# Kernel tuning notes

Measured on AMD Instinct MI355X. Metric: run time of the kernel, lower is better.

## Reference

```python
import jax, jax.numpy as jnp
import numpy as np

S, P, H, E = 32, 32, 128, 64        # scenes, peds/scene, h_dim, embedding_dim
B1, B2 = 512, 1024                  # mlp_pre_pool hidden, bottleneck_dim
M1 = 1024                           # decoder mlp hidden
N = S * P
T = 12                              # seq_len (decode horizon)
BN_INV = 1.0 / np.sqrt(1.0 + 1e-5)  # eval-mode BatchNorm, running mean=0 var=1


def setup_inputs() -> dict:
    key = jax.random.key(0)
    ks = jax.random.split(key, 32)
    rn = lambda k, sh, s=0.05: jax.random.normal(k, sh, dtype=jnp.float32) * s
    inp = {
        'last_pos': rn(ks[0], (N, 2), 1.0),
        'last_pos_rel': rn(ks[1], (N, 2), 1.0),
        'h0': rn(ks[2], (N, H), 0.1),
        'c0': rn(ks[3], (N, H), 0.1),
        'seq_start_end': jnp.stack([jnp.arange(S) * P, (jnp.arange(S) + 1) * P], 1).astype(jnp.int32),
        # decoder spatial embedding Linear(2, E)
        'emb_W': rn(ks[4], (E, 2)), 'emb_b': rn(ks[5], (E,)),
        # LSTM (torch gate order i,f,g,o)
        'lstm_Wih': rn(ks[6], (4 * H, E)), 'lstm_Whh': rn(ks[7], (4 * H, H)),
        'lstm_bih': rn(ks[8], (4 * H,)), 'lstm_bhh': rn(ks[9], (4 * H,)),
        # hidden2pos Linear(H, 2)
        'pos_W': rn(ks[10], (2, H)), 'pos_b': rn(ks[11], (2,)),
        # pool_net spatial embedding Linear(2, E)
        'sp_W': rn(ks[12], (E, 2)), 'sp_b': rn(ks[13], (E,)),
        # mlp_pre_pool: Linear(E+H, 512)+BN+ReLU, Linear(512, 1024)+BN+ReLU
        'pp1_W': rn(ks[14], (B1, E + H)), 'pp1_b': rn(ks[15], (B1,)),
        'pp1_g': 1.0 + rn(ks[16], (B1,)), 'pp1_be': rn(ks[17], (B1,)),
        'pp2_W': rn(ks[18], (B2, B1)), 'pp2_b': rn(ks[19], (B2,)),
        'pp2_g': 1.0 + rn(ks[20], (B2,)), 'pp2_be': rn(ks[21], (B2,)),
        # decoder mlp: Linear(H+1024, 1024)+BN+ReLU, Linear(1024, H)+BN+ReLU
        'm1_W': rn(ks[22], (M1, H + B2)), 'm1_b': rn(ks[23], (M1,)),
        'm1_g': 1.0 + rn(ks[24], (M1,)), 'm1_be': rn(ks[25], (M1,)),
        'm2_W': rn(ks[26], (H, M1)), 'm2_b': rn(ks[27], (H,)),
        'm2_g': 1.0 + rn(ks[28], (H,)), 'm2_be': rn(ks[29], (H,)),
    }
    return inp


def _bn(x, g, b):
    return x * BN_INV * g + b


def reference(last_pos, last_pos_rel, h0, c0, seq_start_end,
              emb_W, emb_b, lstm_Wih, lstm_Whh, lstm_bih, lstm_bhh,
              pos_W, pos_b, sp_W, sp_b,
              pp1_W, pp1_b, pp1_g, pp1_be, pp2_W, pp2_b, pp2_g, pp2_be,
              m1_W, m1_b, m1_g, m1_be, m2_W, m2_b, m2_g, m2_be):
    # seq_start_end encodes uniform scenes of size P; pooling is done per scene.
    def step(carry, _):
        h, c, lp, din = carry  # h,c:[N,H]  lp:[N,2]  din:[N,E]
        gates = din @ lstm_Wih.T + lstm_bih + h @ lstm_Whh.T + lstm_bhh
        i, f, g_, o = jnp.split(gates, 4, axis=-1)
        c2 = jax.nn.sigmoid(f) * c + jax.nn.sigmoid(i) * jnp.tanh(g_)
        h2 = jax.nn.sigmoid(o) * jnp.tanh(c2)
        rel_pos = h2 @ pos_W.T + pos_b          # [N,2]
        curr = rel_pos + lp                     # [N,2]
        # ---- PoolHiddenNet: per-scene all-pairs gather -> MLP -> max ----
        ps = curr.reshape(S, P, 2)
        rel = ps[:, None, :, :] - ps[:, :, None, :]   # [s,i,j] = pos_j - pos_i
        rel = rel / jnp.maximum(jnp.linalg.norm(rel, axis=-1, keepdims=True), 1e-12)
        emb = rel @ sp_W.T + sp_b                      # [S,P,P,E]
        hj = jnp.broadcast_to(h2.reshape(S, 1, P, H), (S, P, P, H))
        x = jnp.concatenate([emb, hj], -1)             # [S,P,P,E+H]
        x = jax.nn.relu(_bn(x @ pp1_W.T + pp1_b, pp1_g, pp1_be))
        x = jax.nn.relu(_bn(x @ pp2_W.T + pp2_b, pp2_g, pp2_be))
        pool = x.max(axis=2).reshape(N, B2)            # max over neighbours j
        # ---- hidden refinement MLP ----
        dh = jnp.concatenate([h2, pool], 1)
        dh = jax.nn.relu(_bn(dh @ m1_W.T + m1_b, m1_g, m1_be))
        dh = jax.nn.relu(_bn(dh @ m2_W.T + m2_b, m2_g, m2_be))
        din2 = rel_pos @ emb_W.T + emb_b
        return (dh, c2, curr, din2), rel_pos

    din0 = last_pos_rel @ emb_W.T + emb_b
    _, preds = jax.lax.scan(step, (h0, c0, last_pos, din0), None, length=T)
    return preds  # [T, N, 2] predicted relative displacements
```

## Files before the change

### kernel.cpp

```cpp
#include <hip/hip_runtime.h>
#include <hip/hip_bf16.h>
#include <math.h>

#define DEVFN __device__ __forceinline__

constexpr float BN_INV = 0.99999500003749971f;

DEVFN float sigm(float x) { return 1.0f / (1.0f + expf(-x)); }

DEVFN unsigned short f2bf(float f) {
    __hip_bfloat16 b = __float2bfloat16(f);
    return *reinterpret_cast<unsigned short*>(&b);
}
DEVFN float bf2f(unsigned short u) {
    unsigned int x = ((unsigned int)u) << 16;
    return *reinterpret_cast<float*>(&x);
}
DEVFN void splitf(float v, unsigned short& h, unsigned short& l) {
    h = f2bf(v);
    l = f2bf(v - bf2f(h));
}
DEVFN unsigned int pack2(unsigned short a, unsigned short b) {
    return (unsigned int)a | ((unsigned int)b << 16);
}

typedef __attribute__((ext_vector_type(8))) short short8;
typedef __attribute__((ext_vector_type(4))) float f32x4;

#define ASYNC_COPY16(gsrc, ldst)                                                            \
    __builtin_amdgcn_global_load_lds((const __attribute__((address_space(1))) unsigned int*)(gsrc), \
                                     (__attribute__((address_space(3))) unsigned int*)(ldst), 16, 0, 0)


__global__ void pre_misc(
    const float* __restrict__ Wih, const float* __restrict__ Whh,
    const float* __restrict__ bih, const float* __restrict__ bhh,
    float* __restrict__ WgT, float* __restrict__ bg,
    const float* __restrict__ pp1W, const float* __restrict__ pp1g,
    float* __restrict__ Wh1T,
    const float* __restrict__ spW, const float* __restrict__ spb,
    const float* __restrict__ pp1b, const float* __restrict__ pp1be,
    float* __restrict__ Mp, float* __restrict__ c1,
    const float* __restrict__ lp, const float* __restrict__ lpr,
    const float* __restrict__ h0, const float* __restrict__ c0,
    const float* __restrict__ embW, const float* __restrict__ embb,
    float* __restrict__ h_st, float* __restrict__ c_st,
    float* __restrict__ curr, float* __restrict__ din) {
    int bid = blockIdx.x, t = threadIdx.x;
    if (bid < 384) {
        int idx = bid * 256 + t;
        int k = idx >> 9, tt = idx & 511;
        WgT[idx] = (k < 64) ? Wih[tt * 64 + k] : Whh[tt * 128 + (k - 64)];
        if (idx < 512) bg[idx] = bih[idx] + bhh[idx];
    } else if (bid < 640) {
        int idx = (bid - 384) * 256 + t;
        int h = idx >> 9, k = idx & 511;
        Wh1T[idx] = pp1W[k * 192 + 64 + h] * (BN_INV * pp1g[k]);
    } else if (bid < 642) {
        int k = (bid - 640) * 256 + t;
        float m0 = 0.f, m1 = 0.f, c0v = 0.f;
        for (int e = 0; e < 64; e++) {
            float w = pp1W[k * 192 + e];
            m0 += spW[e * 2] * w; m1 += spW[e * 2 + 1] * w; c0v += spb[e] * w;
        }
        float s = BN_INV * pp1g[k];
        Mp[k] = m0 * s; Mp[512 + k] = m1 * s;
        c1[k] = (c0v + pp1b[k]) * s + pp1be[k];
    } else {
        int idx = (bid - 642) * 256 + t;
        h_st[idx] = h0[idx];
        c_st[idx] = c0[idx];
        if (idx < 1024 * 2) curr[idx] = lp[idx];
        if (idx < 1024 * 64) {
            int n = idx >> 6, e = idx & 63;
            din[idx] = fmaf(lpr[n * 2], embW[e * 2], fmaf(lpr[n * 2 + 1], embW[e * 2 + 1], embb[e]));
        }
    }
}

__global__ void pre_w2bf(const float* __restrict__ W, const float* __restrict__ b,
                         const float* __restrict__ g, const float* __restrict__ be,
                         unsigned short* __restrict__ Wbf, float* __restrict__ cv, int swz) {
    int idx = blockIdx.x * blockDim.x + threadIdx.x;
    int ko = idx >> 9, k = idx & 511;
    float s = BN_INV * g[ko];
    int outk = swz ? ((k & ~63) | ((((k >> 3) & 7) ^ (ko & 7)) << 3) | (k & 7)) : k;
    Wbf[(ko << 9) + outk] = f2bf(W[idx] * s);
    if (idx < 1024) cv[idx] = b[idx] * s + be[idx];
}

__global__ void pre_w1split(const float* __restrict__ W, const float* __restrict__ b,
                            const float* __restrict__ g, const float* __restrict__ be,
                            unsigned short* __restrict__ Wh, unsigned short* __restrict__ Wl,
                            float* __restrict__ cv) {
    int idx = blockIdx.x * blockDim.x + threadIdx.x;
    int ko = idx / 1152;
    float s = BN_INV * g[ko];
    unsigned short h, l;
    splitf(W[idx] * s, h, l);
    Wh[idx] = h; Wl[idx] = l;
    if (idx < 1024) {
        float s2 = BN_INV * g[idx];
        cv[idx] = b[idx] * s2 + be[idx];
    }
}

__global__ void pre_w2split(const float* __restrict__ W, const float* __restrict__ b,
                            const float* __restrict__ g, const float* __restrict__ be,
                            unsigned short* __restrict__ Wh, unsigned short* __restrict__ Wl,
                            float* __restrict__ cv) {
    int idx = blockIdx.x * blockDim.x + threadIdx.x;
    int ko = idx >> 10;
    float s = BN_INV * g[ko];
    unsigned short h, l;
    splitf(W[idx] * s, h, l);
    Wh[idx] = h; Wl[idx] = l;
    if (idx < 128) {
        float s2 = BN_INV * g[idx];
        cv[idx] = b[idx] * s2 + be[idx];
    }
}


__global__ __launch_bounds__(512) void k_lstm(
    const float* __restrict__ WgT, const float* __restrict__ bg,
    float* __restrict__ h_st, float* __restrict__ c_st,
    float* __restrict__ din, float* __restrict__ curr,
    unsigned short* __restrict__ h2h, unsigned short* __restrict__ h2l,
    const float* __restrict__ posW, const float* __restrict__ posb,
    const float* __restrict__ embW, const float* __restrict__ embb,
    const float* __restrict__ Wh1T, const float* __restrict__ c1,
    float* __restrict__ Hp, int doHp,
    float* __restrict__ preds) {
    int n0 = blockIdx.x << 2;
    int t = threadIdx.x;
    __shared__ float xs[4][256];
    __shared__ float gates[4][512];
    __shared__ float h2s[4][128];
    __shared__ float rp[4][2];
#pragma unroll
    for (int u = 0; u < 2; u++) {
        int lin = t + (u << 9);
        int r = lin >> 8, k = lin & 255;
        float v = 0.f;
        if (k < 64) v = din[(n0 + r) * 64 + k];
        else if (k < 192) v = h_st[(n0 + r) * 128 + (k - 64)];
        xs[r][k] = v;
    }
    __syncthreads();
    float a0 = bg[t], a1 = a0, a2 = a0, a3 = a0;
#pragma unroll 4
    for (int k = 0; k < 192; k++) {
        float w = WgT[(k << 9) + t];
        a0 = fmaf(xs[0][k], w, a0);
        a1 = fmaf(xs[1][k], w, a1);
        a2 = fmaf(xs[2][k], w, a2);
        a3 = fmaf(xs[3][k], w, a3);
    }
    gates[0][t] = a0; gates[1][t] = a1; gates[2][t] = a2; gates[3][t] = a3;
    __syncthreads();
    {
        int r = t >> 7, hx = t & 127;
        float ig = sigm(gates[r][hx]);
        float fg = sigm(gates[r][128 + hx]);
        float gg = tanhf(gates[r][256 + hx]);
        float og = sigm(gates[r][384 + hx]);
        float c2 = fmaf(fg, c_st[(n0 + r) * 128 + hx], ig * gg);
        float h2 = og * tanhf(c2);
        c_st[(n0 + r) * 128 + hx] = c2;
        unsigned short sh, sl;
        splitf(h2, sh, sl);
        h2h[(n0 + r) * 128 + hx] = sh;
        h2l[(n0 + r) * 128 + hx] = sl;
        h2s[r][hx] = h2;
    }
    __syncthreads();
    int wv = t >> 6, l = t & 63;
    if (wv < 4) {
        float p0 = fmaf(h2s[wv][l], posW[l], h2s[wv][l + 64] * posW[l + 64]);
        float p1 = fmaf(h2s[wv][l], posW[128 + l], h2s[wv][l + 64] * posW[192 + l]);
#pragma unroll
        for (int off = 32; off > 0; off >>= 1) {
            p0 += __shfl_down(p0, off, 64);
            p1 += __shfl_down(p1, off, 64);
        }
        if (l == 0) { rp[wv][0] = p0 + posb[0]; rp[wv][1] = p1 + posb[1]; }
    }
    __syncthreads();
    if (t < 256) {
        int r = t >> 6, e = t & 63;
        float r0 = rp[r][0], r1 = rp[r][1];
        din[(n0 + r) * 64 + e] = fmaf(r0, embW[e * 2], fmaf(r1, embW[e * 2 + 1], embb[e]));
        if (e == 0) {
            preds[(n0 + r) * 2] = r0; preds[(n0 + r) * 2 + 1] = r1;
            curr[(n0 + r) * 2] += r0; curr[(n0 + r) * 2 + 1] += r1;
        }
    }
    if (doHp) {
        float cc = c1[t];
        float q0 = cc, q1 = cc, q2 = cc, q3 = cc;
#pragma unroll 4
        for (int h = 0; h < 128; h++) {
            float w = Wh1T[(h << 9) + t];
            q0 = fmaf(h2s[0][h], w, q0);
            q1 = fmaf(h2s[1][h], w, q1);
            q2 = fmaf(h2s[2][h], w, q2);
            q3 = fmaf(h2s[3][h], w, q3);
        }
        Hp[((n0 + 0) << 9) + t] = q0;
        Hp[((n0 + 1) << 9) + t] = q1;
        Hp[((n0 + 2) << 9) + t] = q2;
        Hp[((n0 + 3) << 9) + t] = q3;
    }
}

__global__ __launch_bounds__(256) void k_x1(
    const float* __restrict__ Hp, const float* __restrict__ Mp,
    const float* __restrict__ curr, unsigned short* __restrict__ x1g) {
    int bid = blockIdx.x;
    int c = bid & 7, q = bid >> 3;
    int i = q & 31, g = q >> 5;
    int s = (g << 3) + c;
    int si = (s << 5) + i;
    int t = threadIdx.x;
    __shared__ float rx[32], ry[32];
    __shared__ float m0s[512], m1s[512];
    for (int u = t; u < 512; u += 256) { m0s[u] = Mp[u]; m1s[u] = Mp[512 + u]; }
    if (t < 32) {
        int jg = (s << 5) + t;
        float dx = curr[jg * 2] - curr[si * 2];
        float dy = curr[jg * 2 + 1] - curr[si * 2 + 1];
        float den = fmaxf(sqrtf(dx * dx + dy * dy), 1e-12f);
        rx[t] = dx / den; ry[t] = dy / den;
    }
    __syncthreads();
    int j = t >> 3, c8 = t & 7;
    float rxv = rx[j], ryv = ry[j];
    const float* hp = Hp + (((s << 5) + j) << 9);
    unsigned short* op = x1g + ((size_t)((si << 5) + j) << 9);
    int swz = (c8 ^ (j & 7)) << 3;
#pragma unroll
    for (int kt = 0; kt < 512; kt += 64) {
        int k = kt + (c8 << 3);
        float4 ha = *(const float4*)(hp + k);
        float4 hb = *(const float4*)(hp + k + 4);
        uint4 o;
        o.x = pack2(f2bf(fmaxf(fmaf(rxv, m0s[k + 0], fmaf(ryv, m1s[k + 0], ha.x)), 0.f)),
                    f2bf(fmaxf(fmaf(rxv, m0s[k + 1], fmaf(ryv, m1s[k + 1], ha.y)), 0.f)));
        o.y = pack2(f2bf(fmaxf(fmaf(rxv, m0s[k + 2], fmaf(ryv, m1s[k + 2], ha.z)), 0.f)),
                    f2bf(fmaxf(fmaf(rxv, m0s[k + 3], fmaf(ryv, m1s[k + 3], ha.w)), 0.f)));
        o.z = pack2(f2bf(fmaxf(fmaf(rxv, m0s[k + 4], fmaf(ryv, m1s[k + 4], hb.x)), 0.f)),
                    f2bf(fmaxf(fmaf(rxv, m0s[k + 5], fmaf(ryv, m1s[k + 5], hb.y)), 0.f)));
        o.w = pack2(f2bf(fmaxf(fmaf(rxv, m0s[k + 6], fmaf(ryv, m1s[k + 6], hb.z)), 0.f)),
                    f2bf(fmaxf(fmaf(rxv, m0s[k + 7], fmaf(ryv, m1s[k + 7], hb.w)), 0.f)));
        *(uint4*)(op + kt + swz) = o;
    }
}

__global__ __launch_bounds__(1024, 4) void k_pool_g(
    const unsigned short* __restrict__ x1g, const unsigned short* __restrict__ W2bf,
    const float* __restrict__ c2v,
    unsigned short* __restrict__ poolh, unsigned short* __restrict__ pooll) {
    int bid = blockIdx.x;
    int c = bid & 7, q = bid >> 3;
    int inner = q & 15, g = q >> 4;
    int s = (g << 3) + c;
    int rb = inner >> 2;
    int koB = (inner & 3) << 8;
    int t = threadIdx.x;
    int lane = t & 63, wv = t >> 6;
    int quad = lane >> 4, l15 = lane & 15;
    int wr = wv >> 2, wc = wv & 3;
    int qrow = wr << 6, qcol = wc << 6;
    __shared__ unsigned short As[2][256 * 64];
    __shared__ unsigned short Bs[2][256 * 64];
    f32x4 acc[4][4];
#pragma unroll
    for (int a = 0; a < 4; a++)
#pragma unroll
        for (int b = 0; b < 4; b++) acc[a][b] = (f32x4){0.f, 0.f, 0.f, 0.f};

    int rlane = lane >> 3;
    int clane = (lane & 7) << 3;
    const unsigned short* gA = x1g + (size_t)((s << 10) + (rb << 8) + (wv << 4) + rlane) * 512 + clane;
    const unsigned short* gB = W2bf + (size_t)(koB + (wv << 4) + rlane) * 512 + clane;
    const unsigned short* pa0 = &As[0][((qrow + l15) << 6) + ((quad ^ (l15 & 7)) << 3)];
    const unsigned short* pb0 = &Bs[0][((qcol + l15) << 6) + ((quad ^ (l15 & 7)) << 3)];
    const unsigned short* pa1 = &As[0][((qrow + l15) << 6) + (((4 + quad) ^ (l15 & 7)) << 3)];
    const unsigned short* pb1 = &Bs[0][((qcol + l15) << 6) + (((4 + quad) ^ (l15 & 7)) << 3)];

#define POOL_STAGE(kt, buf)                                           \
    do {                                                              \
        unsigned short* lA = &As[buf][wv << 10];                      \
        unsigned short* lB = &Bs[buf][wv << 10];                      \
        ASYNC_COPY16(gA + (kt), lA);                                  \
        ASYNC_COPY16(gA + (kt) + 8 * 512, lA + (8 << 6));             \
        ASYNC_COPY16(gB + (kt), lB);                                  \
        ASYNC_COPY16(gB + (kt) + 8 * 512, lB + (8 << 6));             \
    } while (0)

    POOL_STAGE(0, 0);
    __syncthreads();
    for (int i = 0; i < 8; i++) {
        if (i < 7) POOL_STAGE((i + 1) << 6, (i + 1) & 1);
        int off = (i & 1) << 14;
        short8 aF[4], bF[4];
#pragma unroll
        for (int a = 0; a < 4; a++) aF[a] = *(const short8*)(pa0 + off + (a << 10));
#pragma unroll
        for (int b = 0; b < 4; b++) bF[b] = *(const short8*)(pb0 + off + (b << 10));
#pragma unroll
        for (int a = 0; a < 4; a++)
#pragma unroll
            for (int b = 0; b < 4; b++)
                acc[a][b] = __builtin_amdgcn_mfma_f32_16x16x32_bf16(aF[a], bF[b], acc[a][b], 0, 0, 0);
#pragma unroll
        for (int a = 0; a < 4; a++) aF[a] = *(const short8*)(pa1 + off + (a << 10));
#pragma unroll
        for (int b = 0; b < 4; b++) bF[b] = *(const short8*)(pb1 + off + (b << 10));
#pragma unroll
        for (int a = 0; a < 4; a++)
#pragma unroll
            for (int b = 0; b < 4; b++)
                acc[a][b] = __builtin_amdgcn_mfma_f32_16x16x32_bf16(aF[a], bF[b], acc[a][b], 0, 0, 0);
        __syncthreads();
    }
#undef POOL_STAGE

    float mx0[4], mx1[4];
#pragma unroll
    for (int b = 0; b < 4; b++) {
        float m = acc[0][b].x;
#pragma unroll
        for (int a = 0; a < 2; a++) {
            m = fmaxf(m, acc[a][b].x); m = fmaxf(m, acc[a][b].y);
            m = fmaxf(m, acc[a][b].z); m = fmaxf(m, acc[a][b].w);
        }
        m = fmaxf(m, __shfl_xor(m, 16));
        m = fmaxf(m, __shfl_xor(m, 32));
        mx0[b] = m;
        float n = acc[2][b].x;
#pragma unroll
        for (int a = 2; a < 4; a++) {
            n = fmaxf(n, acc[a][b].x); n = fmaxf(n, acc[a][b].y);
            n = fmaxf(n, acc[a][b].z); n = fmaxf(n, acc[a][b].w);
        }
        n = fmaxf(n, __shfl_xor(n, 16));
        n = fmaxf(n, __shfl_xor(n, 32));
        mx1[b] = n;
    }
    float v0 = (quad == 0) ? mx0[0] : (quad == 1) ? mx0[1] : (quad == 2) ? mx0[2] : mx0[3];
    float v1 = (quad == 0) ? mx1[0] : (quad == 1) ? mx1[1] : (quad == 2) ? mx1[2] : mx1[3];
    int col = koB + qcol + (quad << 4) + l15;
    int i0 = (rb << 3) + (wr << 1);
    int si0 = (s << 5) + i0;
    float bias = c2v[col];
    float w0 = fmaxf(v0 + bias, 0.f);
    float w1 = fmaxf(v1 + bias, 0.f);
    unsigned short h0, l0, h1, l1;
    splitf(w0, h0, l0); splitf(w1, h1, l1);
    poolh[si0 * 1024 + col] = h0; pooll[si0 * 1024 + col] = l0;
    poolh[(si0 + 1) * 1024 + col] = h1; pooll[(si0 + 1) * 1024 + col] = l1;
}

__global__ __launch_bounds__(256) void k_pool_mfma(
    const float* __restrict__ Hp, const float* __restrict__ Mp,
    const unsigned short* __restrict__ W2bf,
    const float* __restrict__ c2v, const float* __restrict__ curr,
    unsigned short* __restrict__ poolh, unsigned short* __restrict__ pooll) {
    int s = blockIdx.z;
    int rb = blockIdx.y;
    int koBase = blockIdx.x << 7;
    int t = threadIdx.x;
    int lane = t & 63, wv = t >> 6;
    int quad = lane >> 4, l15 = lane & 15;
    int qrow = (wv >> 1) << 6;
    int qcol = (wv & 1) << 6;

    __shared__ unsigned short As[128 * 40];
    __shared__ unsigned short Bs[128 * 40];
    __shared__ float rx[128], ry[128];

    if (t < 128) {
        int iL = t >> 5, j = t & 31;
        int ig = (s << 5) + (rb << 2) + iL;
        int jg = (s << 5) + j;
        float dx = curr[jg * 2] - curr[ig * 2];
        float dy = curr[jg * 2 + 1] - curr[ig * 2 + 1];
        float den = fmaxf(sqrtf(dx * dx + dy * dy), 1e-12f);
        rx[t] = dx / den; ry[t] = dy / den;
    }
    __syncthreads();

    f32x4 acc[4][4];
#pragma unroll
    for (int a = 0; a < 4; a++)
#pragma unroll
        for (int b = 0; b < 4; b++) acc[a][b] = (f32x4){0.f, 0.f, 0.f, 0.f};

    int r0 = t >> 3, c4 = (t & 7) << 2;
    int bn = t >> 1, bk = (t & 1) << 4;

    for (int kt = 0; kt < 512; kt += 32) {
#pragma unroll
        for (int p = 0; p < 4; p++) {
            int rr = r0 + (p << 5);
            int j = rr & 31;
            int kg = kt + c4;
            float4 hv = *(const float4*)(Hp + (((s << 5) + j) << 9) + kg);
            float4 m0 = *(const float4*)(Mp + kg);
            float4 m1 = *(const float4*)(Mp + 512 + kg);
            float rxv = rx[rr], ryv = ry[rr];
            float v0 = fmaxf(fmaf(rxv, m0.x, fmaf(ryv, m1.x, hv.x)), 0.f);
            float v1 = fmaxf(fmaf(rxv, m0.y, fmaf(ryv, m1.y, hv.y)), 0.f);
            float v2 = fmaxf(fmaf(rxv, m0.z, fmaf(ryv, m1.z, hv.z)), 0.f);
            float v3 = fmaxf(fmaf(rxv, m0.w, fmaf(ryv, m1.w, hv.w)), 0.f);
            unsigned int u0 = pack2(f2bf(v0), f2bf(v1));
            unsigned int u1 = pack2(f2bf(v2), f2bf(v3));
            *(uint2*)(&As[rr * 40 + c4]) = make_uint2(u0, u1);
        }
        {
            const unsigned short* src = W2bf + (((koBase + bn) << 9) + kt + bk);
            uint4 w0 = *(const uint4*)src;
            uint4 w1 = *(const uint4*)(src + 8);
            *(uint4*)(&Bs[bn * 40 + bk]) = w0;
            *(uint4*)(&Bs[bn * 40 + bk + 8]) = w1;
        }
        __syncthreads();
        short8 bF[4];
#pragma unroll
        for (int b = 0; b < 4; b++)
            bF[b] = *(const short8*)(&Bs[(qcol + (b << 4) + l15) * 40 + (quad << 3)]);
#pragma unroll
        for (int a = 0; a < 4; a++) {
            short8 aF = *(const short8*)(&As[(qrow + (a << 4) + l15) * 40 + (quad << 3)]);
#pragma unroll
            for (int b = 0; b < 4; b++)
                acc[a][b] = __builtin_amdgcn_mfma_f32_16x16x32_bf16(aF, bF[b], acc[a][b], 0, 0, 0);
        }
        __syncthreads();
    }

    float mx0[4], mx1[4];
#pragma unroll
    for (int b = 0; b < 4; b++) {
        float m = acc[0][b].x;
#pragma unroll
        for (int a = 0; a < 2; a++) {
            m = fmaxf(m, acc[a][b].x); m = fmaxf(m, acc[a][b].y);
            m = fmaxf(m, acc[a][b].z); m = fmaxf(m, acc[a][b].w);
        }
        m = fmaxf(m, __shfl_xor(m, 16));
        m = fmaxf(m, __shfl_xor(m, 32));
        mx0[b] = m;
        float n = acc[2][b].x;
#pragma unroll
        for (int a = 2; a < 4; a++) {
            n = fmaxf(n, acc[a][b].x); n = fmaxf(n, acc[a][b].y);
            n = fmaxf(n, acc[a][b].z); n = fmaxf(n, acc[a][b].w);
        }
        n = fmaxf(n, __shfl_xor(n, 16));
        n = fmaxf(n, __shfl_xor(n, 32));
        mx1[b] = n;
    }
    float v0 = (quad == 0) ? mx0[0] : (quad == 1) ? mx0[1] : (quad == 2) ? mx0[2] : mx0[3];
    float v1 = (quad == 0) ? mx1[0] : (quad == 1) ? mx1[1] : (quad == 2) ? mx1[2] : mx1[3];
    int col = koBase + qcol + (quad << 4) + l15;
    int i0 = (rb << 2) + ((wv >> 1) << 1);
    int si0 = (s << 5) + i0;
    float bias = c2v[col];
    float w0 = fmaxf(v0 + bias, 0.f);
    float w1 = fmaxf(v1 + bias, 0.f);
    unsigned short h0, l0, h1, l1;
    splitf(w0, h0, l0); splitf(w1, h1, l1);
    poolh[si0 * 1024 + col] = h0; pooll[si0 * 1024 + col] = l0;
    poolh[(si0 + 1) * 1024 + col] = h1; pooll[(si0 + 1) * 1024 + col] = l1;
}

__global__ __launch_bounds__(256) void k_m1_mfma(
    const unsigned short* __restrict__ h2h, const unsigned short* __restrict__ h2l,
    const unsigned short* __restrict__ poolh, const unsigned short* __restrict__ pooll,
    const unsigned short* __restrict__ M1h, const unsigned short* __restrict__ M1l,
    const float* __restrict__ cm1,
    unsigned short* __restrict__ dh1h, unsigned short* __restrict__ dh1l) {
    int rowBase = blockIdx.y << 6;
    int koBase = blockIdx.x << 6;
    int t = threadIdx.x;
    int lane = t & 63, wv = t >> 6;
    int quad = lane >> 4, l15 = lane & 15;
    int qrow = (wv >> 1) << 5, qcol = (wv & 1) << 5;
    __shared__ unsigned short Ah[64 * 72], Al[64 * 72], Bh[64 * 72], Bl[64 * 72];
    f32x4 acc[2][2];
#pragma unroll
    for (int a = 0; a < 2; a++)
#pragma unroll
        for (int b = 0; b < 2; b++) acc[a][b] = (f32x4){0.f, 0.f, 0.f, 0.f};

    int ar = t >> 2, ak = (t & 3) << 4;

    for (int kt = 0; kt < 1152; kt += 64) {
        {
            const unsigned short* sH;
            const unsigned short* sL;
            int off;
            if (kt < 128) {
                off = (rowBase + ar) * 128 + kt + ak;
                sH = h2h; sL = h2l;
            } else {
                off = (rowBase + ar) * 1024 + (kt - 128) + ak;
                sH = poolh; sL = pooll;
            }
            *(uint4*)&Ah[ar * 72 + ak] = *(const uint4*)(sH + off);
            *(uint4*)&Ah[ar * 72 + ak + 8] = *(const uint4*)(sH + off + 8);
            *(uint4*)&Al[ar * 72 + ak] = *(const uint4*)(sL + off);
            *(uint4*)&Al[ar * 72 + ak + 8] = *(const uint4*)(sL + off + 8);
        }
        {
            int boff = (koBase + ar) * 1152 + kt + ak;
            *(uint4*)&Bh[ar * 72 + ak] = *(const uint4*)(M1h + boff);
            *(uint4*)&Bh[ar * 72 + ak + 8] = *(const uint4*)(M1h + boff + 8);
            *(uint4*)&Bl[ar * 72 + ak] = *(const uint4*)(M1l + boff);
            *(uint4*)&Bl[ar * 72 + ak + 8] = *(const uint4*)(M1l + boff + 8);
        }
        __syncthreads();
#pragma unroll
        for (int kk2 = 0; kk2 < 2; kk2++) {
            int kc = ((kk2 << 2) | quad) << 3;
            short8 bH[2], bL[2];
#pragma unroll
            for (int b = 0; b < 2; b++) {
                int boff = (qcol + (b << 4) + l15) * 72 + kc;
                bH[b] = *(const short8*)(&Bh[boff]);
                bL[b] = *(const short8*)(&Bl[boff]);
            }
#pragma unroll
            for (int a = 0; a < 2; a++) {
                int aoff = (qrow + (a << 4) + l15) * 72 + kc;
                short8 aH = *(const short8*)(&Ah[aoff]);
                short8 aL = *(const short8*)(&Al[aoff]);
#pragma unroll
                for (int b = 0; b < 2; b++) {
                    acc[a][b] = __builtin_amdgcn_mfma_f32_16x16x32_bf16(aH, bH[b], acc[a][b], 0, 0, 0);
                    acc[a][b] = __builtin_amdgcn_mfma_f32_16x16x32_bf16(aH, bL[b], acc[a][b], 0, 0, 0);
                    acc[a][b] = __builtin_amdgcn_mfma_f32_16x16x32_bf16(aL, bH[b], acc[a][b], 0, 0, 0);
                }
            }
        }
        __syncthreads();
    }
#pragma unroll
    for (int b = 0; b < 2; b++) {
        int col = koBase + qcol + (b << 4) + l15;
        float bias = cm1[col];
#pragma unroll
        for (int a = 0; a < 2; a++) {
#pragma unroll
            for (int rg = 0; rg < 4; rg++) {
                int row = rowBase + qrow + (a << 4) + (quad << 2) + rg;
                float v = fmaxf(acc[a][b][rg] + bias, 0.f);
                unsigned short sh, sl;
                splitf(v, sh, sl);
                dh1h[row * 1024 + col] = sh;
                dh1l[row * 1024 + col] = sl;
            }
        }
    }
}

__global__ __launch_bounds__(256) void k_m2_mfma(
    const unsigned short* __restrict__ dh1h, const unsigned short* __restrict__ dh1l,
    const unsigned short* __restrict__ M2h, const unsigned short* __restrict__ M2l,
    const float* __restrict__ cm2, float* __restrict__ h_st) {
    int rowBase = blockIdx.x << 5;
    int t = threadIdx.x;
    int lane = t & 63, wv = t >> 6;
    int quad = lane >> 4, l15 = lane & 15;
    int qrow = (wv >> 1) << 4;
    int qcol = (wv & 1) << 6;
    __shared__ unsigned short Ah[32 * 40], Al[32 * 40], Bh[128 * 40], Bl[128 * 40];
    f32x4 acc[4];
#pragma unroll
    for (int b = 0; b < 4; b++) acc[b] = (f32x4){0.f, 0.f, 0.f, 0.f};

    int ar = t >> 3, ak = (t & 7) << 2;
    int br = t >> 1, bk = (t & 1) << 4;

    for (int kt = 0; kt < 1024; kt += 32) {
        {
            int off = (rowBase + ar) * 1024 + kt + ak;
            *(uint2*)&Ah[ar * 40 + ak] = *(const uint2*)(dh1h + off);
            *(uint2*)&Al[ar * 40 + ak] = *(const uint2*)(dh1l + off);
        }
        {
            int off = br * 1024 + kt + bk;
            *(uint4*)&Bh[br * 40 + bk] = *(const uint4*)(M2h + off);
            *(uint4*)&Bh[br * 40 + bk + 8] = *(const uint4*)(M2h + off + 8);
            *(uint4*)&Bl[br * 40 + bk] = *(const uint4*)(M2l + off);
            *(uint4*)&Bl[br * 40 + bk + 8] = *(const uint4*)(M2l + off + 8);
        }
        __syncthreads();
        {
            int aoff = (qrow + l15) * 40 + (quad << 3);
            short8 aH = *(const short8*)(&Ah[aoff]);
            short8 aL = *(const short8*)(&Al[aoff]);
#pragma unroll
            for (int b = 0; b < 4; b++) {
                int boff = (qcol + (b << 4) + l15) * 40 + (quad << 3);
                short8 bH = *(const short8*)(&Bh[boff]);
                short8 bL = *(const short8*)(&Bl[boff]);
                acc[b] = __builtin_amdgcn_mfma_f32_16x16x32_bf16(aH, bH, acc[b], 0, 0, 0);
                acc[b] = __builtin_amdgcn_mfma_f32_16x16x32_bf16(aH, bL, acc[b], 0, 0, 0);
                acc[b] = __builtin_amdgcn_mfma_f32_16x16x32_bf16(aL, bH, acc[b], 0, 0, 0);
            }
        }
        __syncthreads();
    }
#pragma unroll
    for (int b = 0; b < 4; b++) {
        int col = qcol + (b << 4) + l15;
        float bias = cm2[col];
#pragma unroll
        for (int rg = 0; rg < 4; rg++) {
            int row = rowBase + qrow + (quad << 2) + rg;
            h_st[row * 128 + col] = fmaxf(acc[b][rg] + bias, 0.f);
        }
    }
}


extern "C" void kernel_launch(void* const* d_in, const int* in_sizes, int n_in,
                              void* d_out, int out_size, void* d_ws, size_t ws_size,
                              hipStream_t stream) {
    const float* last_pos     = (const float*)d_in[0];
    const float* last_pos_rel = (const float*)d_in[1];
    const float* h0   = (const float*)d_in[2];
    const float* c0   = (const float*)d_in[3];
    const float* emb_W = (const float*)d_in[5];
    const float* emb_b = (const float*)d_in[6];
    const float* lstm_Wih = (const float*)d_in[7];
    const float* lstm_Whh = (const float*)d_in[8];
    const float* lstm_bih = (const float*)d_in[9];
    const float* lstm_bhh = (const float*)d_in[10];
    const float* pos_W = (const float*)d_in[11];
    const float* pos_b = (const float*)d_in[12];
    const float* sp_W  = (const float*)d_in[13];
    const float* sp_b  = (const float*)d_in[14];
    const float* pp1_W = (const float*)d_in[15];
    const float* pp1_b = (const float*)d_in[16];
    const float* pp1_g = (const float*)d_in[17];
    const float* pp1_be= (const float*)d_in[18];
    const float* pp2_W = (const float*)d_in[19];
    const float* pp2_b = (const float*)d_in[20];
    const float* pp2_g = (const float*)d_in[21];
    const float* pp2_be= (const float*)d_in[22];
    const float* m1_W  = (const float*)d_in[23];
    const float* m1_b  = (const float*)d_in[24];
    const float* m1_g  = (const float*)d_in[25];
    const float* m1_be = (const float*)d_in[26];
    const float* m2_W  = (const float*)d_in[27];
    const float* m2_b  = (const float*)d_in[28];
    const float* m2_g  = (const float*)d_in[29];
    const float* m2_be = (const float*)d_in[30];
    float* out = (float*)d_out;

    float* p = (float*)d_ws;
    float* WgT  = p; p += 192 * 512;
    float* bg   = p; p += 512;
    float* Wh1T = p; p += 128 * 512;
    float* Mp   = p; p += 2 * 512;
    float* c1   = p; p += 512;
    unsigned short* W2bf = (unsigned short*)p; p += 512 * 1024 / 2;
    float* c2v  = p; p += 1024;
    unsigned short* M1h = (unsigned short*)p; p += 1024 * 1152 / 2;
    unsigned short* M1l = (unsigned short*)p; p += 1024 * 1152 / 2;
    float* cm1  = p; p += 1024;
    unsigned short* M2h = (unsigned short*)p; p += 128 * 1024 / 2;
    unsigned short* M2l = (unsigned short*)p; p += 128 * 1024 / 2;
    float* cm2  = p; p += 128;
    float* h_st = p; p += 1024 * 128;
    float* c_st = p; p += 1024 * 128;
    unsigned short* h2h = (unsigned short*)p; p += 1024 * 128 / 2;
    unsigned short* h2l = (unsigned short*)p; p += 1024 * 128 / 2;
    float* curr = p; p += 1024 * 2;
    float* din  = p; p += 1024 * 64;
    float* Hp   = p; p += 1024 * 512;
    unsigned short* poolh = (unsigned short*)p; p += 1024 * 1024 / 2;
    unsigned short* pooll = (unsigned short*)p; p += 1024 * 1024 / 2;
    unsigned short* dh1h = (unsigned short*)p; p += 1024 * 1024 / 2;
    unsigned short* dh1l = (unsigned short*)p; p += 1024 * 1024 / 2;
    unsigned short* x1g = (unsigned short*)p;
    size_t need = (size_t)((char*)(x1g + (size_t)32768 * 512) - (char*)d_ws);
    int big = (ws_size >= need) ? 1 : 0;

    pre_misc<<<1154, 256, 0, stream>>>(lstm_Wih, lstm_Whh, lstm_bih, lstm_bhh, WgT, bg,
                                       pp1_W, pp1_g, Wh1T,
                                       sp_W, sp_b, pp1_b, pp1_be, Mp, c1,
                                       last_pos, last_pos_rel, h0, c0, emb_W, emb_b,
                                       h_st, c_st, curr, din);
    pre_w2bf<<<2048, 256, 0, stream>>>(pp2_W, pp2_b, pp2_g, pp2_be, W2bf, c2v, big);
    pre_w1split<<<4608, 256, 0, stream>>>(m1_W, m1_b, m1_g, m1_be, M1h, M1l, cm1);
    pre_w2split<<<512, 256, 0, stream>>>(m2_W, m2_b, m2_g, m2_be, M2h, M2l, cm2);

    for (int t = 0; t < 12; t++) {
        k_lstm<<<256, 512, 0, stream>>>(WgT, bg, h_st, c_st, din, curr, h2h, h2l,
                                        pos_W, pos_b, emb_W, emb_b,
                                        Wh1T, c1, Hp, (t < 11) ? 1 : 0, out + t * 2048);
        if (t == 11) break;
        if (big) {
            k_x1<<<1024, 256, 0, stream>>>(Hp, Mp, curr, x1g);
            k_pool_g<<<512, 1024, 0, stream>>>(x1g, W2bf, c2v, poolh, pooll);
        } else {
            k_pool_mfma<<<dim3(8, 8, 32), 256, 0, stream>>>(Hp, Mp, W2bf, c2v, curr,
                                                            poolh, pooll);
        }
        k_m1_mfma<<<dim3(16, 16), 256, 0, stream>>>(h2h, h2l, poolh, pooll,
                                                    M1h, M1l, cm1, dh1h, dh1l);
        k_m2_mfma<<<32, 256, 0, stream>>>(dh1h, dh1l, M2h, M2l, cm2, h_st);
    }
}
```

Measured before the change: 1.387 ms.

## Prefetch tiles into registers in m1/m2 GEMMs, retile m2, fuse weight prep

Merges the three weight-preparation kernels into one launch. The m1 GEMM now prefetches the next k-tile into registers while computing the current one, and its blocks are remapped so each XCD-sized group of 8 blocks shares weight columns. The m2 GEMM is retiled from 32 blocks of 32x128 to 128 blocks of 16x64 with the same register prefetch, so more CUs are used. The aim is to hide global-load latency and improve occupancy, at the cost of more registers per thread and more redundant loads of A tiles in m2.

```diff
diff --git a/kernel.cpp b/kernel.cpp
--- a/kernel.cpp
+++ b/kernel.cpp
@@ -78,46 +78,48 @@
     }
 }
 
-__global__ void pre_w2bf(const float* __restrict__ W, const float* __restrict__ b,
-                         const float* __restrict__ g, const float* __restrict__ be,
-                         unsigned short* __restrict__ Wbf, float* __restrict__ cv, int swz) {
-    int idx = blockIdx.x * blockDim.x + threadIdx.x;
-    int ko = idx >> 9, k = idx & 511;
-    float s = BN_INV * g[ko];
-    int outk = swz ? ((k & ~63) | ((((k >> 3) & 7) ^ (ko & 7)) << 3) | (k & 7)) : k;
-    Wbf[(ko << 9) + outk] = f2bf(W[idx] * s);
-    if (idx < 1024) cv[idx] = b[idx] * s + be[idx];
-}
-
-__global__ void pre_w1split(const float* __restrict__ W, const float* __restrict__ b,
-                            const float* __restrict__ g, const float* __restrict__ be,
-                            unsigned short* __restrict__ Wh, unsigned short* __restrict__ Wl,
-                            float* __restrict__ cv) {
-    int idx = blockIdx.x * blockDim.x + threadIdx.x;
-    int ko = idx / 1152;
-    float s = BN_INV * g[ko];
-    unsigned short h, l;
-    splitf(W[idx] * s, h, l);
-    Wh[idx] = h; Wl[idx] = l;
-    if (idx < 1024) {
-        float s2 = BN_INV * g[idx];
-        cv[idx] = b[idx] * s2 + be[idx];
-    }
-}
-
-__global__ void pre_w2split(const float* __restrict__ W, const float* __restrict__ b,
-                            const float* __restrict__ g, const float* __restrict__ be,
-                            unsigned short* __restrict__ Wh, unsigned short* __restrict__ Wl,
-                            float* __restrict__ cv) {
-    int idx = blockIdx.x * blockDim.x + threadIdx.x;
-    int ko = idx >> 10;
-    float s = BN_INV * g[ko];
-    unsigned short h, l;
-    splitf(W[idx] * s, h, l);
-    Wh[idx] = h; Wl[idx] = l;
-    if (idx < 128) {
-        float s2 = BN_INV * g[idx];
-        cv[idx] = b[idx] * s2 + be[idx];
+__global__ void pre_w(
+    const float* __restrict__ pp2W, const float* __restrict__ pp2b,
+    const float* __restrict__ pp2g, const float* __restrict__ pp2be,
+    unsigned short* __restrict__ W2bf, float* __restrict__ c2v, int swz,
+    const float* __restrict__ m1W, const float* __restrict__ m1b,
+    const float* __restrict__ m1g, const float* __restrict__ m1be,
+    unsigned short* __restrict__ M1h, unsigned short* __restrict__ M1l,
+    float* __restrict__ cm1,
+    const float* __restrict__ m2W, const float* __restrict__ m2b,
+    const float* __restrict__ m2g, const float* __restrict__ m2be,
+    unsigned short* __restrict__ M2h, unsigned short* __restrict__ M2l,
+    float* __restrict__ cm2) {
+    int bid = blockIdx.x, t = threadIdx.x;
+    if (bid < 2048) {
+        int idx = bid * 256 + t;
+        int ko = idx >> 9, k = idx & 511;
+        float s = BN_INV * pp2g[ko];
+        int outk = swz ? ((k & ~63) | ((((k >> 3) & 7) ^ (ko & 7)) << 3) | (k & 7)) : k;
+        W2bf[(ko << 9) + outk] = f2bf(pp2W[idx] * s);
+        if (idx < 1024) c2v[idx] = pp2b[idx] * s + pp2be[idx];
+    } else if (bid < 6656) {
+        int idx = (bid - 2048) * 256 + t;
+        int ko = idx / 1152;
+        float s = BN_INV * m1g[ko];
+        unsigned short h, l;
+        splitf(m1W[idx] * s, h, l);
+        M1h[idx] = h; M1l[idx] = l;
+        if (idx < 1024) {
+            float s2 = BN_INV * m1g[idx];
+            cm1[idx] = m1b[idx] * s2 + m1be[idx];
+        }
+    } else {
+        int idx = (bid - 6656) * 256 + t;
+        int ko = idx >> 10;
+        float s = BN_INV * m2g[ko];
+        unsigned short h, l;
+        splitf(m2W[idx] * s, h, l);
+        M2h[idx] = h; M2l[idx] = l;
+        if (idx < 128) {
+            float s2 = BN_INV * m2g[idx];
+            cm2[idx] = m2b[idx] * s2 + m2be[idx];
+        }
     }
 }
 
@@ -483,8 +485,12 @@
     const unsigned short* __restrict__ M1h, const unsigned short* __restrict__ M1l,
     const float* __restrict__ cm1,
     unsigned short* __restrict__ dh1h, unsigned short* __restrict__ dh1l) {
-    int rowBase = blockIdx.y << 6;
-    int koBase = blockIdx.x << 6;
+    int bid = blockIdx.x;
+    int c = bid & 7, q = bid >> 3;
+    int kg = (c << 1) | (q >> 4);
+    int rowg = q & 15;
+    int rowBase = rowg << 6;
+    int koBase = kg << 6;
     int t = threadIdx.x;
     int lane = t & 63, wv = t >> 6;
     int quad = lane >> 4, l15 = lane & 15;
@@ -497,32 +503,29 @@
         for (int b = 0; b < 2; b++) acc[a][b] = (f32x4){0.f, 0.f, 0.f, 0.f};
 
     int ar = t >> 2, ak = (t & 3) << 4;
-
-    for (int kt = 0; kt < 1152; kt += 64) {
-        {
-            const unsigned short* sH;
-            const unsigned short* sL;
-            int off;
-            if (kt < 128) {
-                off = (rowBase + ar) * 128 + kt + ak;
-                sH = h2h; sL = h2l;
-            } else {
-                off = (rowBase + ar) * 1024 + (kt - 128) + ak;
-                sH = poolh; sL = pooll;
-            }
-            *(uint4*)&Ah[ar * 72 + ak] = *(const uint4*)(sH + off);
-            *(uint4*)&Ah[ar * 72 + ak + 8] = *(const uint4*)(sH + off + 8);
-            *(uint4*)&Al[ar * 72 + ak] = *(const uint4*)(sL + off);
-            *(uint4*)&Al[ar * 72 + ak + 8] = *(const uint4*)(sL + off + 8);
-        }
-        {
-            int boff = (koBase + ar) * 1152 + kt + ak;
-            *(uint4*)&Bh[ar * 72 + ak] = *(const uint4*)(M1h + boff);
-            *(uint4*)&Bh[ar * 72 + ak + 8] = *(const uint4*)(M1h + boff + 8);
-            *(uint4*)&Bl[ar * 72 + ak] = *(const uint4*)(M1l + boff);
-            *(uint4*)&Bl[ar * 72 + ak + 8] = *(const uint4*)(M1l + boff + 8);
-        }
+    uint4 pf[8];
+
+#define M1_LOAD(kt)                                                           \
+    do {                                                                      \
+        const unsigned short *sH, *sL;                                        \
+        int off;                                                              \
+        if ((kt) < 128) { off = (rowBase + ar) * 128 + (kt) + ak; sH = h2h; sL = h2l; } \
+        else { off = (rowBase + ar) * 1024 + ((kt) - 128) + ak; sH = poolh; sL = pooll; } \
+        pf[0] = *(const uint4*)(sH + off);   pf[1] = *(const uint4*)(sH + off + 8); \
+        pf[2] = *(const uint4*)(sL + off);   pf[3] = *(const uint4*)(sL + off + 8); \
+        int boff = (koBase + ar) * 1152 + (kt) + ak;                          \
+        pf[4] = *(const uint4*)(M1h + boff); pf[5] = *(const uint4*)(M1h + boff + 8); \
+        pf[6] = *(const uint4*)(M1l + boff); pf[7] = *(const uint4*)(M1l + boff + 8); \
+    } while (0)
+
+    M1_LOAD(0);
+    for (int i = 0; i < 18; i++) {
+        *(uint4*)&Ah[ar * 72 + ak] = pf[0]; *(uint4*)&Ah[ar * 72 + ak + 8] = pf[1];
+        *(uint4*)&Al[ar * 72 + ak] = pf[2]; *(uint4*)&Al[ar * 72 + ak + 8] = pf[3];
+        *(uint4*)&Bh[ar * 72 + ak] = pf[4]; *(uint4*)&Bh[ar * 72 + ak + 8] = pf[5];
+        *(uint4*)&Bl[ar * 72 + ak] = pf[6]; *(uint4*)&Bl[ar * 72 + ak + 8] = pf[7];
         __syncthreads();
+        if (i < 17) M1_LOAD((i + 1) << 6);
 #pragma unroll
         for (int kk2 = 0; kk2 < 2; kk2++) {
             int kc = ((kk2 << 2) | quad) << 3;
@@ -548,6 +551,7 @@
         }
         __syncthreads();
     }
+#undef M1_LOAD
 #pragma unroll
     for (int b = 0; b < 2; b++) {
         int col = koBase + qcol + (b << 4) + l15;
@@ -571,59 +575,57 @@
     const unsigned short* __restrict__ dh1h, const unsigned short* __restrict__ dh1l,
     const unsigned short* __restrict__ M2h, const unsigned short* __restrict__ M2l,
     const float* __restrict__ cm2, float* __restrict__ h_st) {
-    int rowBase = blockIdx.x << 5;
+    int bid = blockIdx.x;
+    int rowBase = (bid >> 1) << 4;
+    int koBase = (bid & 1) << 6;
     int t = threadIdx.x;
     int lane = t & 63, wv = t >> 6;
     int quad = lane >> 4, l15 = lane & 15;
-    int qrow = (wv >> 1) << 4;
-    int qcol = (wv & 1) << 6;
-    __shared__ unsigned short Ah[32 * 40], Al[32 * 40], Bh[128 * 40], Bl[128 * 40];
-    f32x4 acc[4];
-#pragma unroll
-    for (int b = 0; b < 4; b++) acc[b] = (f32x4){0.f, 0.f, 0.f, 0.f};
-
-    int ar = t >> 3, ak = (t & 7) << 2;
-    int br = t >> 1, bk = (t & 1) << 4;
-
-    for (int kt = 0; kt < 1024; kt += 32) {
-        {
-            int off = (rowBase + ar) * 1024 + kt + ak;
-            *(uint2*)&Ah[ar * 40 + ak] = *(const uint2*)(dh1h + off);
-            *(uint2*)&Al[ar * 40 + ak] = *(const uint2*)(dh1l + off);
-        }
-        {
-            int off = br * 1024 + kt + bk;
-            *(uint4*)&Bh[br * 40 + bk] = *(const uint4*)(M2h + off);
-            *(uint4*)&Bh[br * 40 + bk + 8] = *(const uint4*)(M2h + off + 8);
-            *(uint4*)&Bl[br * 40 + bk] = *(const uint4*)(M2l + off);
-            *(uint4*)&Bl[br * 40 + bk + 8] = *(const uint4*)(M2l + off + 8);
-        }
+    int qcol = wv << 4;
+    __shared__ unsigned short Ah[16 * 40], Al[16 * 40], Bh[64 * 40], Bl[64 * 40];
+    f32x4 acc = (f32x4){0.f, 0.f, 0.f, 0.f};
+
+    int ar = t >> 4, ak = (t & 15) << 1;
+    int br = t >> 2, bk = (t & 3) << 3;
+    unsigned int pa0, pa1;
+    uint4 pb0, pb1;
+
+#define M2_LOAD(kt)                                                 \
+    do {                                                            \
+        int aoff = (rowBase + ar) * 1024 + (kt) + ak;               \
+        pa0 = *(const unsigned int*)(dh1h + aoff);                  \
+        pa1 = *(const unsigned int*)(dh1l + aoff);                  \
+        int boff = (koBase + br) * 1024 + (kt) + bk;                \
+        pb0 = *(const uint4*)(M2h + boff);                          \
+        pb1 = *(const uint4*)(M2l + boff);                          \
+    } while (0)
+
+    M2_LOAD(0);
+    for (int i = 0; i < 32; i++) {
+        *(unsigned int*)&Ah[ar * 40 + ak] = pa0;
+        *(unsigned int*)&Al[ar * 40 + ak] = pa1;
+        *(uint4*)&Bh[br * 40 + bk] = pb0;
+        *(uint4*)&Bl[br * 40 + bk] = pb1;
         __syncthreads();
-        {
-            int aoff = (qrow + l15) * 40 + (quad << 3);
-            short8 aH = *(const short8*)(&Ah[aoff]);
-            short8 aL = *(const short8*)(&Al[aoff]);
-#pragma unroll
-            for (int b = 0; b < 4; b++) {
-                int boff = (qcol + (b << 4) + l15) * 40 + (quad << 3);
-                short8 bH = *(const short8*)(&Bh[boff]);
-                short8 bL = *(const short8*)(&Bl[boff]);
-                acc[b] = __builtin_amdgcn_mfma_f32_16x16x32_bf16(aH, bH, acc[b], 0, 0, 0);
-                acc[b] = __builtin_amdgcn_mfma_f32_16x16x32_bf16(aH, bL, acc[b], 0, 0, 0);
-                acc[b] = __builtin_amdgcn_mfma_f32_16x16x32_bf16(aL, bH, acc[b], 0, 0, 0);
-            }
-        }
+        if (i < 31) M2_LOAD((i + 1) << 5);
+        int aoff2 = l15 * 40 + (quad << 3);
+        short8 aH = *(const short8*)(&Ah[aoff2]);
+        short8 aL = *(const short8*)(&Al[aoff2]);
+        int boff2 = (qcol + l15) * 40 + (quad << 3);
+        short8 bH = *(const short8*)(&Bh[boff2]);
+        short8 bL = *(const short8*)(&Bl[boff2]);
+        acc = __builtin_amdgcn_mfma_f32_16x16x32_bf16(aH, bH, acc, 0, 0, 0);
+        acc = __builtin_amdgcn_mfma_f32_16x16x32_bf16(aH, bL, acc, 0, 0, 0);
+        acc = __builtin_amdgcn_mfma_f32_16x16x32_bf16(aL, bH, acc, 0, 0, 0);
         __syncthreads();
     }
-#pragma unroll
-    for (int b = 0; b < 4; b++) {
-        int col = qcol + (b << 4) + l15;
-        float bias = cm2[col];
-#pragma unroll
-        for (int rg = 0; rg < 4; rg++) {
-            int row = rowBase + qrow + (quad << 2) + rg;
-            h_st[row * 128 + col] = fmaxf(acc[b][rg] + bias, 0.f);
-        }
+#undef M2_LOAD
+    int col = koBase + qcol + l15;
+    float bias = cm2[col];
+#pragma unroll
+    for (int rg = 0; rg < 4; rg++) {
+        int row = rowBase + (quad << 2) + rg;
+        h_st[row * 128 + col] = fmaxf(acc[rg] + bias, 0.f);
     }
 }
 
@@ -697,9 +699,9 @@
                                        sp_W, sp_b, pp1_b, pp1_be, Mp, c1,
                                        last_pos, last_pos_rel, h0, c0, emb_W, emb_b,
                                        h_st, c_st, curr, din);
-    pre_w2bf<<<2048, 256, 0, stream>>>(pp2_W, pp2_b, pp2_g, pp2_be, W2bf, c2v, big);
-    pre_w1split<<<4608, 256, 0, stream>>>(m1_W, m1_b, m1_g, m1_be, M1h, M1l, cm1);
-    pre_w2split<<<512, 256, 0, stream>>>(m2_W, m2_b, m2_g, m2_be, M2h, M2l, cm2);
+    pre_w<<<7168, 256, 0, stream>>>(pp2_W, pp2_b, pp2_g, pp2_be, W2bf, c2v, big,
+                                    m1_W, m1_b, m1_g, m1_be, M1h, M1l, cm1,
+                                    m2_W, m2_b, m2_g, m2_be, M2h, M2l, cm2);
 
     for (int t = 0; t < 12; t++) {
         k_lstm<<<256, 512, 0, stream>>>(WgT, bg, h_st, c_st, din, curr, h2h, h2l,
@@ -713,8 +715,8 @@
             k_pool_mfma<<<dim3(8, 8, 32), 256, 0, stream>>>(Hp, Mp, W2bf, c2v, curr,
                                                             poolh, pooll);
         }
-        k_m1_mfma<<<dim3(16, 16), 256, 0, stream>>>(h2h, h2l, poolh, pooll,
-                                                    M1h, M1l, cm1, dh1h, dh1l);
-        k_m2_mfma<<<32, 256, 0, stream>>>(dh1h, dh1l, M2h, M2l, cm2, h_st);
-    }
-}
+        k_m1_mfma<<<256, 256, 0, stream>>>(h2h, h2l, poolh, pooll,
+                                           M1h, M1l, cm1, dh1h, dh1l);
+        k_m2_mfma<<<128, 256, 0, stream>>>(dh1h, dh1l, M2h, M2l, cm2, h_st);
+    }
+}
```

Result: slower. 1.529 ms (+10.2%).
